# Kernel tuning notes

Measured on AMD Instinct MI355X. Metric: run time of the kernel, lower is better.

The kernel has to match this reference:

```python
import jax, jax.numpy as jnp
import numpy as np
from jax import lax

B, L, S = 32, 513, 1024
H, HEADS, NCLS = 512, 4, 128
SPACE, PAD, EOS = 1, 0, 2
WORD = 8                 # chunk: 7 phones + 1 space
WPB = (L - 1) // WORD    # words per batch = 64
TOTAL_WORDS = B * WPB    # 2048
WLEN = WORD - 1          # 7


def setup_inputs() -> dict:
    key = jax.random.key(0)
    ks = jax.random.split(key, 22)
    # targets: phones in [3, NCLS), every WORD-th token after position 0 is SPACE; no EOS/PAD
    tg = np.array(jax.random.randint(ks[0], (B, L), 3, NCLS))
    t = np.arange(1, L)
    col = tg[:, 1:]
    col[:, (t - 1) % WORD == WORD - 1] = SPACE
    tg[:, 1:] = col
    targets = jnp.asarray(tg, dtype=jnp.int32)
    sc = 0.02
    p = lambda k, shape: jax.random.normal(k, shape, jnp.float32) * sc
    return dict(
        targets=targets,
        encoder_outputs=jax.random.normal(ks[1], (B, S, H), jnp.float32),
        emb_w=p(ks[2], (NCLS, H)),
        w_ih0=p(ks[3], (4 * H, H)), w_hh0=p(ks[4], (4 * H, H)),
        b_ih0=p(ks[5], (4 * H,)), b_hh0=p(ks[6], (4 * H,)),
        w_ih1=p(ks[7], (4 * H, H)), w_hh1=p(ks[8], (4 * H, H)),
        b_ih1=p(ks[9], (4 * H,)), b_hh1=p(ks[10], (4 * H,)),
        q_w=p(ks[11], (H, H)), q_b=p(ks[12], (H,)),
        k_w=p(ks[13], (H, H)), k_b=p(ks[14], (H,)),
        v_w=p(ks[15], (H, H)), v_b=p(ks[16], (H,)),
        fc1_w=p(ks[17], (H, 2 * H)), fc1_b=p(ks[18], (H,)),
        fc2_w=p(ks[19], (NCLS, H)), fc2_b=p(ks[20], (NCLS,)),
    )


def lstm_layer(x, w_ih, w_hh, b_ih, b_hh):
    # PyTorch LSTM, gate order (i, f, g, o), batch_first
    Bx, _, _ = x.shape
    Hh = w_hh.shape[1]
    xp = jnp.einsum('bth,gh->btg', x, w_ih) + b_ih + b_hh  # [B,T,4H]
    def step(carry, xt):
        h, c = carry
        g = xt + h @ w_hh.T
        i, f, gg, o = jnp.split(g, 4, axis=-1)
        c = jax.nn.sigmoid(f) * c + jax.nn.sigmoid(i) * jnp.tanh(gg)
        h = jax.nn.sigmoid(o) * jnp.tanh(c)
        return (h, c), h
    init = (jnp.zeros((Bx, Hh), x.dtype), jnp.zeros((Bx, Hh), x.dtype))
    _, hs = lax.scan(step, init, xp.transpose(1, 0, 2))
    return hs.transpose(1, 0, 2)


def mha(q_in, kv, q_w, q_b, k_w, k_b, v_w, v_b):
    dh = H // HEADS
    q = (q_in @ q_w.T + q_b).reshape(B, -1, HEADS, dh)
    k = (kv @ k_w.T + k_b).reshape(B, -1, HEADS, dh)
    v = (kv @ v_w.T + v_b).reshape(B, -1, HEADS, dh)
    scores = jnp.einsum('bqhd,bkhd->bhqk', q, k) / jnp.sqrt(jnp.float32(dh))
    attn = jax.nn.softmax(scores, axis=-1)
    ctx = jnp.einsum('bhqk,bkhd->bqhd', attn, v).reshape(B, -1, H)
    return ctx, attn


def split_words(ids, feat):
    # vectorized _split_output_to_word: segment-ids + scatter instead of python loops
    T = ids.shape[1]
    D = feat.shape[-1]
    boundary = (ids == SPACE) | (ids == PAD)          # word delimiters
    word_id = jnp.cumsum(boundary, axis=1) - boundary  # exclusive cumsum
    tpos = jnp.arange(T)
    seed = jnp.where(boundary, tpos + 1, 0)
    start = jnp.concatenate([jnp.zeros((B, 1), seed.dtype), lax.cummax(seed, axis=1)[:, :-1]], axis=1)
    pos = jnp.clip(tpos - start, 0, WLEN - 1)          # position within word
    gidx = jnp.where(boundary, TOTAL_WORDS, jnp.arange(B)[:, None] * WPB + word_id)
    out = jnp.zeros((TOTAL_WORDS + 1, WLEN, D), feat.dtype)
    out = out.at[gidx.ravel(), pos.ravel()].set(feat.reshape(-1, D))
    return out[:TOTAL_WORDS]  # [2048, 7, 2H]; all words length WLEN so torch zero-pad is a no-op


def reference(targets, encoder_outputs, emb_w, w_ih0, w_hh0, b_ih0, b_hh0, w_ih1, w_hh1, b_ih1, b_hh1, q_w, q_b, k_w, k_b, v_w, v_b, fc1_w, fc1_b, fc2_w, fc2_b):
    input_rnn = targets  # targets contain no eos by construction, so the eos-filter view is identity
    embedded = emb_w[input_rnn]  # input_dropout is identity in eval mode
    x = lstm_layer(embedded, w_ih0, w_hh0, b_ih0, b_hh0)
    outputs = lstm_layer(x, w_ih1, w_hh1, b_ih1, b_hh1)
    context, attn = mha(outputs, encoder_outputs, q_w, q_b, k_w, k_b, v_w, v_b)
    feat = jnp.concatenate([embedded[:, 1:], context[:, :-1]], axis=-1)  # [B, L-1, 2H]
    mis = split_words(input_rnn[:, 1:], feat)
    cat = jnp.concatenate([outputs, context], axis=-1)  # [B, L, 2H]
    h1 = jnp.tanh(cat @ fc1_w.T + fc1_b)
    logits = h1 @ fc2_w.T + fc2_b
    logp = jax.nn.log_softmax(logits, axis=-1)  # [B, L, NCLS]
    return logp, attn, mis
```

## Files before the change

### kernel.cpp

```cpp
#include <hip/hip_runtime.h>


typedef __attribute__((ext_vector_type(8))) short bf16x8;
typedef __attribute__((ext_vector_type(4))) float f32x4;

union U128 { unsigned long long q[2]; bf16x8 v; };

__device__ __forceinline__ unsigned short f2bf(float f) {
  union { float f; unsigned int u; } v; v.f = f;
  unsigned int r = (v.u + 0x7fffu + ((v.u >> 16) & 1u)) >> 16;
  return (unsigned short)r;
}
__device__ __forceinline__ float bf2f(unsigned short h) {
  union { unsigned int u; float f; } v; v.u = ((unsigned int)h) << 16;
  return v.f;
}

__device__ __forceinline__ unsigned long long ld_dev(const unsigned short* p) {
  return __hip_atomic_load((const unsigned long long*)p, __ATOMIC_RELAXED,
                           __HIP_MEMORY_SCOPE_AGENT);
}
__device__ __forceinline__ void st_dev(unsigned short* p, unsigned long long x) {
  __hip_atomic_store((unsigned long long*)p, x, __ATOMIC_RELAXED,
                     __HIP_MEMORY_SCOPE_AGENT);
}

typedef const __attribute__((address_space(1))) void* gp1_t;
typedef __attribute__((address_space(3))) void* lp3_t;
__device__ __forceinline__ void glds16(const void* g, void* s) {
  __builtin_amdgcn_global_load_lds((gp1_t)g, (lp3_t)s, 16, 0, 0);
}

struct Gemm {
  const unsigned short* A; const unsigned short* W; const float* bias;
  float* C1; unsigned short* C2;
  long lda, ldw, ldc1, ldc2;
  long zA, zAh, zW, zWh, zC1, zC1h, zC2, zC2h;
  long M, Mclamp;
  int N, K, heads, act;
  float alpha;
};

__global__ __launch_bounds__(256, 2) void gemm_bt(Gemm g) {
  __shared__ unsigned short aSh[128 * 32];
  __shared__ unsigned short bSh[128 * 32];
  const int tid = threadIdx.x;
  const int wave = tid >> 6, lane = tid & 63;
  const int zb = blockIdx.z / g.heads, zh = blockIdx.z % g.heads;
  const unsigned short* A = g.A + (long)zb * g.zA + (long)zh * g.zAh;
  const unsigned short* W = g.W + (long)zb * g.zW + (long)zh * g.zWh;
  const long mBlk = (long)blockIdx.y * 128;
  const long nBlk = (long)blockIdx.x * 128;
  const int sRow = wave * 16 + (lane >> 2);
  const int sCol = (lane & 3) * 8;
  long ar0 = mBlk + sRow;      if (ar0 > g.Mclamp) ar0 = g.Mclamp;
  long ar1 = mBlk + 64 + sRow; if (ar1 > g.Mclamp) ar1 = g.Mclamp;
  const unsigned short* gA0 = A + ar0 * g.lda + sCol;
  const unsigned short* gA1 = A + ar1 * g.lda + sCol;
  const unsigned short* gW0 = W + (nBlk + sRow) * g.ldw + sCol;
  const unsigned short* gW1 = W + (nBlk + 64 + sRow) * g.ldw + sCol;
  unsigned short* sA0 = aSh + wave * 512;
  unsigned short* sA1 = aSh + 2048 + wave * 512;
  unsigned short* sB0 = bSh + wave * 512;
  unsigned short* sB1 = bSh + 2048 + wave * 512;
  f32x4 acc[4][4] = {};
  const int wm = wave & 1, wn = wave >> 1;
  const int fm = lane & 15, fq = lane >> 4;
  for (int k0 = 0; k0 < g.K; k0 += 32) {
    glds16(gA0 + k0, sA0);
    glds16(gA1 + k0, sA1);
    glds16(gW0 + k0, sB0);
    glds16(gW1 + k0, sB1);
    __syncthreads();
    bf16x8 af[4], bfr[4];
#pragma unroll
    for (int i = 0; i < 4; ++i)
      af[i] = *(const bf16x8*)(aSh + (wm * 64 + i * 16 + fm) * 32 + fq * 8);
#pragma unroll
    for (int j = 0; j < 4; ++j)
      bfr[j] = *(const bf16x8*)(bSh + (wn * 64 + j * 16 + fm) * 32 + fq * 8);
#pragma unroll
    for (int i = 0; i < 4; ++i)
#pragma unroll
      for (int j = 0; j < 4; ++j)
        acc[i][j] = __builtin_amdgcn_mfma_f32_16x16x32_bf16(af[i], bfr[j], acc[i][j], 0, 0, 0);
    __syncthreads();
  }
  float* C1 = g.C1 ? g.C1 + (long)zb * g.zC1 + (long)zh * g.zC1h : nullptr;
  unsigned short* C2 = g.C2 ? g.C2 + (long)zb * g.zC2 + (long)zh * g.zC2h : nullptr;
#pragma unroll
  for (int j = 0; j < 4; ++j) {
    long n = nBlk + wn * 64 + j * 16 + fm;
    float bias = g.bias ? g.bias[n] : 0.f;
#pragma unroll
    for (int i = 0; i < 4; ++i) {
      long mBase = mBlk + wm * 64 + i * 16 + fq * 4;
#pragma unroll
      for (int r = 0; r < 4; ++r) {
        long m = mBase + r;
        if (m < g.M) {
          float v = acc[i][j][r] * g.alpha + bias;
          if (g.act) v = tanhf(v);
          if (C1) C1[m * g.ldc1 + n] = v;
          if (C2) C2[m * g.ldc2 + n] = f2bf(v);
        }
      }
    }
  }
}

__global__ __launch_bounds__(256, 1) void lstm_fused(
    const float* __restrict__ xp,
    const unsigned short* __restrict__ wih1,
    const unsigned short* __restrict__ whh0,
    const unsigned short* __restrict__ whh1,
    const float* __restrict__ bias1,
    unsigned short* __restrict__ h0,
    unsigned short* __restrict__ h1,
    unsigned int* bar) {
  __shared__ unsigned short wSh[2 * 16 * 520];
  __shared__ float gS[1056];
  __shared__ __align__(16) unsigned short hStage[256];
  const int tid = threadIdx.x, lane = tid & 63, wave = tid >> 6;
  const int bx = blockIdx.x;
  const int fm = lane & 15, fq = lane >> 4;

  if (bx < 64) {
    const int j0 = bx * 8;
    {
      const int row = tid >> 3, cb = (tid & 7) * 64;
      const unsigned short* wsrc =
          whh0 + ((long)((row >> 3) * 512 + j0 + (row & 7))) * 512 + cb;
      unsigned short* dst = wSh + row * 520 + cb;
#pragma unroll
      for (int c = 0; c < 64; c += 8) *(bf16x8*)(dst + c) = *(const bf16x8*)(wsrc + c);
    }
    __syncthreads();
    const int wm = wave & 1, wn = wave >> 1;
    const unsigned short* wrow = wSh + (wn * 16 + fm) * 520 + fq * 8;
    const long ab = wm * 16 + fm;
    const int cb2 = tid >> 3, jl = tid & 7;
    const float* xpp = xp + (long)cb2 * 513 * 2048 + j0 + jl;
    float cSt = 0.f;
    for (int r = 0; r < 514; ++r) {
      if (r < 513) {
        const int t = r;
        const float* xq = xpp + (long)t * 2048;
        float x0 = xq[0], x1 = xq[512], x2 = xq[1024], x3 = xq[1536];
        f32x4 acc = {0.f, 0.f, 0.f, 0.f};
        if (t > 0) {
          U128 afr[16];
          const unsigned short* hr = h0 + (ab * 513 + (t - 1)) * 512 + fq * 8;
#pragma unroll
          for (int kk = 0; kk < 16; ++kk) {
            afr[kk].q[0] = ld_dev(hr + kk * 32);
            afr[kk].q[1] = ld_dev(hr + kk * 32 + 4);
          }
#pragma unroll
          for (int kk = 0; kk < 16; ++kk)
            acc = __builtin_amdgcn_mfma_f32_16x16x32_bf16(
                afr[kk].v, *(const bf16x8*)(wrow + kk * 32), acc, 0, 0, 0);
        }
#pragma unroll
        for (int rr = 0; rr < 4; ++rr)
          gS[(wn * 16 + fm) * 33 + wm * 16 + fq * 4 + rr] = acc[rr];
        __syncthreads();
        {
          float gi = gS[jl * 33 + cb2] + x0;
          float gf = gS[(8 + jl) * 33 + cb2] + x1;
          float gg = gS[(16 + jl) * 33 + cb2] + x2;
          float go = gS[(24 + jl) * 33 + cb2] + x3;
          float ig = 1.f / (1.f + __expf(-gi));
          float fg = 1.f / (1.f + __expf(-gf));
          float og = 1.f / (1.f + __expf(-go));
          cSt = fg * cSt + ig * tanhf(gg);
          hStage[tid] = f2bf(og * tanhf(cSt));
        }
        __syncthreads();
        if (tid < 64) {
          const int b2 = tid >> 1, half = tid & 1;
          unsigned long long q = *(const unsigned long long*)(hStage + b2 * 8 + half * 4);
          st_dev(h0 + ((long)b2 * 513 + t) * 512 + j0 + half * 4, q);
        }
      }
      if (r < 513) {
        __syncthreads();
        if (tid == 0) {
          __hip_atomic_fetch_add(bar + (bx & 7) * 1024, 1u, __ATOMIC_RELAXED,
                                 __HIP_MEMORY_SCOPE_AGENT);
          const unsigned int tgt = 192u * (unsigned)(r + 1);
          for (;;) {
            unsigned int s = 0;
#pragma unroll
            for (int i = 0; i < 8; ++i)
              s += __hip_atomic_load(bar + i * 1024, __ATOMIC_RELAXED,
                                     __HIP_MEMORY_SCOPE_AGENT);
            if (s >= tgt) break;
            __builtin_amdgcn_s_sleep(1);
          }
        }
        __syncthreads();
      }
    }
  } else {
    const int j0 = (bx - 64) * 4;
    {
      const int mat = tid >> 7, row = (tid >> 3) & 15, cb = (tid & 7) * 64;
      const unsigned short* wsrc = (mat ? whh1 : wih1) +
          ((long)((row >> 2) * 512 + j0 + (row & 3))) * 512 + cb;
      unsigned short* dst = wSh + (mat * 16 + row) * 520 + cb;
#pragma unroll
      for (int c = 0; c < 64; c += 8) *(bf16x8*)(dst + c) = *(const bf16x8*)(wsrc + c);
    }
    __syncthreads();
    const int wm = wave & 1, ws = wave >> 1;
    const unsigned short* wrow = wSh + (ws * 16 + fm) * 520 + fq * 8;
    const long ab = wm * 16 + fm;
    const int cb2 = tid >> 2, jl = tid & 3;
    float bv0 = 0.f, bv1 = 0.f, bv2 = 0.f, bv3 = 0.f;
    if (tid < 128) {
      bv0 = bias1[j0 + jl];
      bv1 = bias1[512 + j0 + jl];
      bv2 = bias1[1024 + j0 + jl];
      bv3 = bias1[1536 + j0 + jl];
    }
    float cSt = 0.f;
    for (int r = 0; r < 514; ++r) {
      if (r >= 1) {
        const int t = r - 1;
        f32x4 acc = {0.f, 0.f, 0.f, 0.f};
        if (ws == 0 || t > 0) {
          U128 afr[16];
          const unsigned short* hr = (ws == 0)
              ? h0 + (ab * 513 + t) * 512 + fq * 8
              : h1 + (ab * 513 + (t - 1)) * 1024 + fq * 8;
#pragma unroll
          for (int kk = 0; kk < 16; ++kk) {
            afr[kk].q[0] = ld_dev(hr + kk * 32);
            afr[kk].q[1] = ld_dev(hr + kk * 32 + 4);
          }
#pragma unroll
          for (int kk = 0; kk < 16; ++kk)
            acc = __builtin_amdgcn_mfma_f32_16x16x32_bf16(
                afr[kk].v, *(const bf16x8*)(wrow + kk * 32), acc, 0, 0, 0);
        }
#pragma unroll
        for (int rr = 0; rr < 4; ++rr)
          gS[(ws * 16 + fm) * 33 + wm * 16 + fq * 4 + rr] = acc[rr];
        __syncthreads();
        if (tid < 128) {
          float gi = gS[jl * 33 + cb2]        + gS[(16 + jl) * 33 + cb2] + bv0;
          float gf = gS[(4 + jl) * 33 + cb2]  + gS[(20 + jl) * 33 + cb2] + bv1;
          float gg = gS[(8 + jl) * 33 + cb2]  + gS[(24 + jl) * 33 + cb2] + bv2;
          float go = gS[(12 + jl) * 33 + cb2] + gS[(28 + jl) * 33 + cb2] + bv3;
          float ig = 1.f / (1.f + __expf(-gi));
          float fg = 1.f / (1.f + __expf(-gf));
          float og = 1.f / (1.f + __expf(-go));
          cSt = fg * cSt + ig * tanhf(gg);
          hStage[tid] = f2bf(og * tanhf(cSt));
        }
        __syncthreads();
        if (tid < 32) {
          unsigned long long q = *(const unsigned long long*)(hStage + tid * 4);
          st_dev(h1 + ((long)tid * 513 + t) * 1024 + j0, q);
        }
      }
      if (r < 513) {
        __syncthreads();
        if (tid == 0) {
          __hip_atomic_fetch_add(bar + (bx & 7) * 1024, 1u, __ATOMIC_RELAXED,
                                 __HIP_MEMORY_SCOPE_AGENT);
          const unsigned int tgt = 192u * (unsigned)(r + 1);
          for (;;) {
            unsigned int s = 0;
#pragma unroll
            for (int i = 0; i < 8; ++i)
              s += __hip_atomic_load(bar + i * 1024, __ATOMIC_RELAXED,
                                     __HIP_MEMORY_SCOPE_AGENT);
            if (s >= tgt) break;
            __builtin_amdgcn_s_sleep(1);
          }
        }
        __syncthreads();
      }
    }
  }
}


struct CastJob { const float* src; unsigned short* dst; long n; };
struct CastJobs { CastJob j[11]; };
__global__ void cast_multi(CastJobs jb) {
  const CastJob j = jb.j[blockIdx.z];
  long n4 = j.n >> 2;
  for (long i = blockIdx.x * (long)blockDim.x + threadIdx.x; i < n4;
       i += (long)gridDim.x * blockDim.x) {
    float4 f = ((const float4*)j.src)[i];
    ushort4 o;
    o.x = f2bf(f.x); o.y = f2bf(f.y); o.z = f2bf(f.z); o.w = f2bf(f.w);
    ((ushort4*)j.dst)[i] = o;
  }
}

__global__ void bias_sum(const float* a0, const float* b0, float* o0,
                         const float* a1, const float* b1, float* o1) {
  int i = blockIdx.x * 256 + threadIdx.x;
  if (i < 2048) { o0[i] = a0[i] + b0[i]; o1[i] = a1[i] + b1[i]; }
}

__global__ __launch_bounds__(256) void embed_gather(const int* __restrict__ tg,
                                                    const unsigned short* __restrict__ emb,
                                                    unsigned short* __restrict__ out) {
  long row = blockIdx.x;
  int id = tg[row];
  const unsigned short* s = emb + (long)id * 512;
  unsigned short* d = out + row * 512;
  int c = threadIdx.x * 2;
  *(ushort2*)(d + c) = *(const ushort2*)(s + c);
}

__global__ void word_map(const int* __restrict__ tg, int* __restrict__ map) {
  int b = threadIdx.x;
  if (b >= 32) return;
  int word_id = 0, start = 0;
  for (int i = 0; i < 512; ++i) {
    int id = tg[b * 513 + i + 1];
    bool bd = (id == 1) || (id == 0);
    if (bd) {
      map[b * 512 + i] = -1;
      word_id++; start = i + 1;
    } else {
      int pos = i - start; if (pos > 6) pos = 6;
      map[b * 512 + i] = (b * 64 + word_id) * 7 + pos;
    }
  }
}

__global__ __launch_bounds__(256) void vtrans(const unsigned short* __restrict__ v,
                                              unsigned short* __restrict__ vt) {
  __shared__ unsigned short tile[64][33];
  const int bh = blockIdx.z, b = bh >> 2, h = bh & 3;
  const int s0 = blockIdx.x * 64, d0 = blockIdx.y * 32;
  const int tid = threadIdx.x;
  {
    const int dd = tid & 31, sb = tid >> 5;
#pragma unroll
    for (int k = 0; k < 8; ++k) {
      int s = sb + k * 8;
      tile[s][dd] = v[((long)b * 1024 + s0 + s) * 512 + h * 128 + d0 + dd];
    }
  }
  __syncthreads();
  {
    const int ss = tid & 63, db = tid >> 6;
#pragma unroll
    for (int k = 0; k < 8; ++k) {
      int d = db + k * 4;
      vt[((long)bh * 128 + d0 + d) * 1024 + s0 + ss] = tile[ss][d];
    }
  }
}

__global__ __launch_bounds__(256) void softmax_row(unsigned short* __restrict__ sc,
                                                   float* __restrict__ attnOut) {
  const long row = blockIdx.x;
  unsigned short* sr = sc + row * 1024;
  const int tid = threadIdx.x, lane = tid & 63, wave = tid >> 6;
  __shared__ float red[8];
  ushort4 raw = *(const ushort4*)(sr + tid * 4);
  float v0 = bf2f(raw.x), v1 = bf2f(raw.y), v2 = bf2f(raw.z), v3 = bf2f(raw.w);
  float m = fmaxf(fmaxf(v0, v1), fmaxf(v2, v3));
  for (int o = 32; o; o >>= 1) m = fmaxf(m, __shfl_down(m, o));
  if (lane == 0) red[wave] = m;
  __syncthreads();
  m = fmaxf(fmaxf(red[0], red[1]), fmaxf(red[2], red[3]));
  float e0 = __expf(v0 - m), e1 = __expf(v1 - m), e2 = __expf(v2 - m), e3 = __expf(v3 - m);
  float s = e0 + e1 + e2 + e3;
  for (int o = 32; o; o >>= 1) s += __shfl_down(s, o);
  if (lane == 0) red[4 + wave] = s;
  __syncthreads();
  float inv = 1.f / (red[4] + red[5] + red[6] + red[7]);
  float a0 = e0 * inv, a1 = e1 * inv, a2 = e2 * inv, a3 = e3 * inv;
  float4 fo; fo.x = a0; fo.y = a1; fo.z = a2; fo.w = a3;
  *(float4*)(attnOut + row * 1024 + tid * 4) = fo;
  ushort4 ob; ob.x = f2bf(a0); ob.y = f2bf(a1); ob.z = f2bf(a2); ob.w = f2bf(a3);
  *(ushort4*)(sr + tid * 4) = ob;
}

__global__ __launch_bounds__(128) void mis_scatter(const int* __restrict__ map,
                                                   const int* __restrict__ tg,
                                                   const float* __restrict__ emb_w,
                                                   const float* __restrict__ ctx,
                                                   float* __restrict__ mis) {
  int bi = blockIdx.x;
  int g = map[bi];
  if (g < 0) return;
  int b = bi >> 9, i = bi & 511;
  float* dst = mis + (long)g * 1024;
  int id = tg[b * 513 + i + 1];
  const float* es = emb_w + (long)id * 512;
  const float* cs = ctx + ((long)b * 513 + i) * 512;
  for (int c = threadIdx.x; c < 512; c += 128) {
    dst[c] = es[c];
    dst[512 + c] = cs[c];
  }
}

__global__ __launch_bounds__(256) void logsoftmax_rows(const float* __restrict__ logits,
                                                       float* __restrict__ out) {
  int row = blockIdx.x * 4 + (threadIdx.x >> 6);
  if (row >= 16416) return;
  int lane = threadIdx.x & 63;
  const float* lr = logits + (long)row * 128;
  float a = lr[lane], b = lr[lane + 64];
  float m = fmaxf(a, b);
  for (int o = 32; o; o >>= 1) m = fmaxf(m, __shfl_down(m, o));
  m = __shfl(m, 0);
  float s = __expf(a - m) + __expf(b - m);
  for (int o = 32; o; o >>= 1) s += __shfl_down(s, o);
  s = __shfl(s, 0);
  float ls = m + __logf(s);
  out[(long)row * 128 + lane] = a - ls;
  out[(long)row * 128 + lane + 64] = b - ls;
}


extern "C" void kernel_launch(void* const* d_in, const int* in_sizes, int n_in,
                              void* d_out, int out_size, void* d_ws, size_t ws_size,
                              hipStream_t stream) {
  (void)in_sizes; (void)n_in; (void)out_size; (void)ws_size;
  const int*   targets = (const int*)d_in[0];
  const float* enc   = (const float*)d_in[1];
  const float* emb_w = (const float*)d_in[2];
  const float* w_ih0 = (const float*)d_in[3];
  const float* w_hh0 = (const float*)d_in[4];
  const float* b_ih0 = (const float*)d_in[5];
  const float* b_hh0 = (const float*)d_in[6];
  const float* w_ih1 = (const float*)d_in[7];
  const float* w_hh1 = (const float*)d_in[8];
  const float* b_ih1 = (const float*)d_in[9];
  const float* b_hh1 = (const float*)d_in[10];
  const float* q_w = (const float*)d_in[11]; const float* q_b = (const float*)d_in[12];
  const float* k_w = (const float*)d_in[13]; const float* k_b = (const float*)d_in[14];
  const float* v_w = (const float*)d_in[15]; const float* v_b = (const float*)d_in[16];
  const float* fc1_w = (const float*)d_in[17]; const float* fc1_b = (const float*)d_in[18];
  const float* fc2_w = (const float*)d_in[19]; const float* fc2_b = (const float*)d_in[20];

  float* out_logp = (float*)d_out;
  float* out_attn = out_logp + 2101248;
  float* out_mis  = out_logp + 69341184;

  char* ws = (char*)d_ws;
  size_t off = 0;
  auto take = [&](size_t bytes) -> char* {
    char* p = ws + off; off += (bytes + 255) & ~(size_t)255; return p;
  };
  unsigned int* bar   = (unsigned int*)take(65536);
  int* map            = (int*)take(65536);
  float* bias0        = (float*)take(8192);
  float* bias1        = (float*)take(8192);
  unsigned short* wih0b = (unsigned short*)take(2097152);
  unsigned short* whh0b = (unsigned short*)take(2097152);
  unsigned short* wih1b = (unsigned short*)take(2097152);
  unsigned short* whh1b = (unsigned short*)take(2097152);
  unsigned short* qwb   = (unsigned short*)take(524288);
  unsigned short* kwb   = (unsigned short*)take(524288);
  unsigned short* vwb   = (unsigned short*)take(524288);
  unsigned short* fc1wb = (unsigned short*)take(1048576);
  unsigned short* fc2wb = (unsigned short*)take(131072);
  unsigned short* embb  = (unsigned short*)take(131072);
  unsigned short* emb_bf = (unsigned short*)take(16908288);
  unsigned short* enc_bf = (unsigned short*)take(33554432);
  float* xp             = (float*)take(135266304);
  unsigned short* scores = (unsigned short*)xp;
  unsigned short* h0_bf = (unsigned short*)take(16908288);
  unsigned short* cat_bf = (unsigned short*)take(33816576);
  unsigned short* q_bf  = (unsigned short*)take(16908288);
  unsigned short* k_bf  = (unsigned short*)take(33554432);
  unsigned short* v_bf  = (unsigned short*)take(33554432);
  unsigned short* v_t   = (unsigned short*)take(33554432);
  float* ctx            = (float*)take(33816576);
  unsigned short* h1_bf = (unsigned short*)take(16908288);
  float* logits         = (float*)take(8454144);

  hipMemsetAsync(bar, 0, 32768, stream);
  hipMemsetAsync(out_mis, 0, (size_t)14680064 * 4, stream);

  CastJobs cj;
  cj.j[0]  = {w_ih0, wih0b, 1048576};
  cj.j[1]  = {w_hh0, whh0b, 1048576};
  cj.j[2]  = {w_ih1, wih1b, 1048576};
  cj.j[3]  = {w_hh1, whh1b, 1048576};
  cj.j[4]  = {q_w,   qwb,   262144};
  cj.j[5]  = {k_w,   kwb,   262144};
  cj.j[6]  = {v_w,   vwb,   262144};
  cj.j[7]  = {fc1_w, fc1wb, 524288};
  cj.j[8]  = {fc2_w, fc2wb, 65536};
  cj.j[9]  = {emb_w, embb,  65536};
  cj.j[10] = {enc,   enc_bf, 16777216};
  cast_multi<<<dim3(256, 1, 11), 256, 0, stream>>>(cj);
  bias_sum<<<8, 256, 0, stream>>>(b_ih0, b_hh0, bias0, b_ih1, b_hh1, bias1);
  word_map<<<1, 64, 0, stream>>>(targets, map);
  embed_gather<<<16416, 256, 0, stream>>>(targets, embb, emb_bf);

  auto launch_gemm = [&](const unsigned short* A, long lda, long zA, long zAh,
                         const unsigned short* W, long ldw, long zW, long zWh,
                         const float* bias, float* C1, long ldc1, long zC1, long zC1h,
                         unsigned short* C2, long ldc2, long zC2, long zC2h,
                         long M, long Mclamp, int N, int K, int heads, int Z,
                         float alpha, int act) {
    Gemm g;
    g.A = A; g.W = W; g.bias = bias; g.C1 = C1; g.C2 = C2;
    g.lda = lda; g.ldw = ldw; g.ldc1 = ldc1; g.ldc2 = ldc2;
    g.zA = zA; g.zAh = zAh; g.zW = zW; g.zWh = zWh;
    g.zC1 = zC1; g.zC1h = zC1h; g.zC2 = zC2; g.zC2h = zC2h;
    g.M = M; g.Mclamp = Mclamp; g.N = N; g.K = K; g.heads = heads;
    g.act = act; g.alpha = alpha;
    dim3 grid((unsigned)(N / 128), (unsigned)((M + 127) / 128), (unsigned)Z);
    gemm_bt<<<grid, 256, 0, stream>>>(g);
  };

  launch_gemm(emb_bf, 512, 0, 0, wih0b, 512, 0, 0, bias0,
              xp, 2048, 0, 0, nullptr, 0, 0, 0,
              16512, 16511, 2048, 512, 1, 1, 1.f, 0);
  lstm_fused<<<192, 256, 0, stream>>>(xp, wih1b, whh0b, whh1b, bias1,
                                      h0_bf, cat_bf, bar);

  launch_gemm(cat_bf, 1024, 0, 0, qwb, 512, 0, 0, q_b,
              nullptr, 0, 0, 0, q_bf, 512, 0, 0,
              16512, 16511, 512, 512, 1, 1, 1.f, 0);
  launch_gemm(enc_bf, 512, 0, 0, kwb, 512, 0, 0, k_b,
              nullptr, 0, 0, 0, k_bf, 512, 0, 0,
              32768, 32767, 512, 512, 1, 1, 1.f, 0);
  launch_gemm(enc_bf, 512, 0, 0, vwb, 512, 0, 0, v_b,
              nullptr, 0, 0, 0, v_bf, 512, 0, 0,
              32768, 32767, 512, 512, 1, 1, 1.f, 0);
  vtrans<<<dim3(16, 4, 128), 256, 0, stream>>>(v_bf, v_t);

  launch_gemm(q_bf, 512, 262656, 128, k_bf, 512, 524288, 128, nullptr,
              nullptr, 0, 0, 0, scores, 1024, 2101248, 525312,
              513, 512, 1024, 128, 4, 128, 0.08838834764831845f, 0);
  softmax_row<<<65664, 256, 0, stream>>>(scores, out_attn);
  launch_gemm(scores, 1024, 2101248, 525312, v_t, 1024, 524288, 131072, nullptr,
              ctx, 512, 262656, 128, cat_bf + 512, 1024, 525312, 128,
              513, 512, 128, 1024, 4, 128, 1.f, 0);
  mis_scatter<<<16384, 128, 0, stream>>>(map, targets, emb_w, ctx, out_mis);

  launch_gemm(cat_bf, 1024, 0, 0, fc1wb, 1024, 0, 0, fc1_b,
              nullptr, 0, 0, 0, h1_bf, 512, 0, 0,
              16512, 16511, 512, 1024, 1, 1, 1.f, 1);
  launch_gemm(h1_bf, 512, 0, 0, fc2wb, 512, 0, 0, fc2_b,
              logits, 128, 0, 0, nullptr, 0, 0, 0,
              16512, 16511, 128, 512, 1, 1, 1.f, 0);
  logsoftmax_rows<<<4104, 256, 0, stream>>>(logits, out_logp);
}
```

Before: 4.035 ms.

## Restructure fused LSTM into 48 blocks with register weights and per-block flags

The persistent two-layer LSTM kernel drops from 192 to 48 blocks. Each wave now holds its weight fragments in registers instead of LDS and computes all four gates for its hidden slice, so the gate nonlinearity runs straight from the MFMA accumulators without an LDS transpose. The global counting barrier is replaced by per-block progress flags. Layer 0 waits only on layer-0 blocks, and layer 1 waits on layer-0 step t and layer-1 step t-1, which lets the two layers pipeline instead of moving in lockstep. The cost is heavy register pressure from 64 bf16x8 fragments per thread and fewer CUs doing the serial work.

```diff
diff --git a/kernel.cpp b/kernel.cpp
--- a/kernel.cpp
+++ b/kernel.cpp
@@ -5,6 +5,7 @@
 typedef __attribute__((ext_vector_type(4))) float f32x4;
 
 union U128 { unsigned long long q[2]; bf16x8 v; };
+union HV { ushort4 u; unsigned long long q; };
 
 __device__ __forceinline__ unsigned short f2bf(float f) {
   union { float f; unsigned int u; } v; v.f = f;
@@ -23,6 +24,12 @@
 __device__ __forceinline__ void st_dev(unsigned short* p, unsigned long long x) {
   __hip_atomic_store((unsigned long long*)p, x, __ATOMIC_RELAXED,
                      __HIP_MEMORY_SCOPE_AGENT);
+}
+__device__ __forceinline__ unsigned int ld_flag(const unsigned int* p) {
+  return __hip_atomic_load(p, __ATOMIC_RELAXED, __HIP_MEMORY_SCOPE_AGENT);
+}
+__device__ __forceinline__ void st_flag(unsigned int* p, unsigned int v) {
+  __hip_atomic_store(p, v, __ATOMIC_RELAXED, __HIP_MEMORY_SCOPE_AGENT);
 }
 
 typedef const __attribute__((address_space(1))) void* gp1_t;
@@ -118,171 +125,182 @@
     unsigned short* __restrict__ h0,
     unsigned short* __restrict__ h1,
     unsigned int* bar) {
-  __shared__ unsigned short wSh[2 * 16 * 520];
-  __shared__ float gS[1056];
-  __shared__ __align__(16) unsigned short hStage[256];
+  __shared__ float xch[16 * 128];
   const int tid = threadIdx.x, lane = tid & 63, wave = tid >> 6;
+  const int fm = lane & 15, fq = lane >> 4;
   const int bx = blockIdx.x;
-  const int fm = lane & 15, fq = lane >> 4;
-
-  if (bx < 64) {
-    const int j0 = bx * 8;
-    {
-      const int row = tid >> 3, cb = (tid & 7) * 64;
-      const unsigned short* wsrc =
-          whh0 + ((long)((row >> 3) * 512 + j0 + (row & 7))) * 512 + cb;
-      unsigned short* dst = wSh + row * 520 + cb;
-#pragma unroll
-      for (int c = 0; c < 64; c += 8) *(bf16x8*)(dst + c) = *(const bf16x8*)(wsrc + c);
-    }
-    __syncthreads();
-    const int wm = wave & 1, wn = wave >> 1;
-    const unsigned short* wrow = wSh + (wn * 16 + fm) * 520 + fq * 8;
-    const long ab = wm * 16 + fm;
-    const int cb2 = tid >> 3, jl = tid & 7;
-    const float* xpp = xp + (long)cb2 * 513 * 2048 + j0 + jl;
-    float cSt = 0.f;
-    for (int r = 0; r < 514; ++r) {
-      if (r < 513) {
-        const int t = r;
-        const float* xq = xpp + (long)t * 2048;
-        float x0 = xq[0], x1 = xq[512], x2 = xq[1024], x3 = xq[1536];
-        f32x4 acc = {0.f, 0.f, 0.f, 0.f};
-        if (t > 0) {
-          U128 afr[16];
-          const unsigned short* hr = h0 + (ab * 513 + (t - 1)) * 512 + fq * 8;
-#pragma unroll
-          for (int kk = 0; kk < 16; ++kk) {
-            afr[kk].q[0] = ld_dev(hr + kk * 32);
-            afr[kk].q[1] = ld_dev(hr + kk * 32 + 4);
+
+  if (bx < 16) {
+    const int j0 = bx * 32;
+    const int m = wave & 1, p = wave >> 1;
+    const int b = m * 16 + fm;
+    const int c0 = p * 16 + fq * 4;
+    bf16x8 wf[4][16];
+#pragma unroll
+    for (int g = 0; g < 4; ++g) {
+      const unsigned short* wr =
+          whh0 + ((long)(g * 512 + j0 + p * 16 + fm)) * 512 + fq * 8;
+#pragma unroll
+      for (int kk = 0; kk < 16; ++kk)
+        wf[g][kk] = *(const bf16x8*)(wr + kk * 32);
+    }
+    const float* xpt = xp + ((long)b * 513) * 2048 + j0 + c0;
+    unsigned short* hout = h0 + ((long)b * 513) * 512 + j0 + c0;
+    const unsigned short* hin = h0 + ((long)b * 513) * 512 + fq * 8;
+    float cS[4] = {0.f, 0.f, 0.f, 0.f};
+#pragma unroll 1
+    for (int t = 0; t < 513; ++t) {
+      const float4 xi = *(const float4*)(xpt + (long)t * 2048);
+      const float4 xf = *(const float4*)(xpt + (long)t * 2048 + 512);
+      const float4 xg = *(const float4*)(xpt + (long)t * 2048 + 1024);
+      const float4 xo = *(const float4*)(xpt + (long)t * 2048 + 1536);
+      if (tid == 0 && t > 0) {
+        for (;;) {
+          unsigned int mn = ~0u;
+#pragma unroll
+          for (int i = 0; i < 16; ++i) {
+            unsigned int v = ld_flag(bar + i * 16);
+            mn = v < mn ? v : mn;
           }
-#pragma unroll
-          for (int kk = 0; kk < 16; ++kk)
-            acc = __builtin_amdgcn_mfma_f32_16x16x32_bf16(
-                afr[kk].v, *(const bf16x8*)(wrow + kk * 32), acc, 0, 0, 0);
-        }
-#pragma unroll
-        for (int rr = 0; rr < 4; ++rr)
-          gS[(wn * 16 + fm) * 33 + wm * 16 + fq * 4 + rr] = acc[rr];
-        __syncthreads();
-        {
-          float gi = gS[jl * 33 + cb2] + x0;
-          float gf = gS[(8 + jl) * 33 + cb2] + x1;
-          float gg = gS[(16 + jl) * 33 + cb2] + x2;
-          float go = gS[(24 + jl) * 33 + cb2] + x3;
+          if (mn >= (unsigned int)t) break;
+          __builtin_amdgcn_s_sleep(1);
+        }
+      }
+      __syncthreads();
+      f32x4 a0 = {}, a1 = {}, a2 = {}, a3 = {};
+      if (t > 0) {
+        U128 hf[16];
+        const unsigned short* hr = hin + (long)(t - 1) * 512;
+#pragma unroll
+        for (int kk = 0; kk < 16; ++kk) {
+          hf[kk].q[0] = ld_dev(hr + kk * 32);
+          hf[kk].q[1] = ld_dev(hr + kk * 32 + 4);
+        }
+#pragma unroll
+        for (int kk = 0; kk < 16; ++kk) {
+          a0 = __builtin_amdgcn_mfma_f32_16x16x32_bf16(wf[0][kk], hf[kk].v, a0, 0, 0, 0);
+          a1 = __builtin_amdgcn_mfma_f32_16x16x32_bf16(wf[1][kk], hf[kk].v, a1, 0, 0, 0);
+          a2 = __builtin_amdgcn_mfma_f32_16x16x32_bf16(wf[2][kk], hf[kk].v, a2, 0, 0, 0);
+          a3 = __builtin_amdgcn_mfma_f32_16x16x32_bf16(wf[3][kk], hf[kk].v, a3, 0, 0, 0);
+        }
+      }
+      const float xiv[4] = {xi.x, xi.y, xi.z, xi.w};
+      const float xfv[4] = {xf.x, xf.y, xf.z, xf.w};
+      const float xgv[4] = {xg.x, xg.y, xg.z, xg.w};
+      const float xov[4] = {xo.x, xo.y, xo.z, xo.w};
+      unsigned short hh[4];
+#pragma unroll
+      for (int rr = 0; rr < 4; ++rr) {
+        float gi = a0[rr] + xiv[rr];
+        float gf = a1[rr] + xfv[rr];
+        float gg = a2[rr] + xgv[rr];
+        float go = a3[rr] + xov[rr];
+        float ig = 1.f / (1.f + __expf(-gi));
+        float fg = 1.f / (1.f + __expf(-gf));
+        float og = 1.f / (1.f + __expf(-go));
+        cS[rr] = fg * cS[rr] + ig * tanhf(gg);
+        hh[rr] = f2bf(og * tanhf(cS[rr]));
+      }
+      HV hv; hv.u.x = hh[0]; hv.u.y = hh[1]; hv.u.z = hh[2]; hv.u.w = hh[3];
+      st_dev(hout + (long)t * 512, hv.q);
+      __syncthreads();
+      if (tid == 0) st_flag(bar + bx * 16, (unsigned int)(t + 1));
+    }
+  } else {
+    const int blk = bx - 16, j0 = blk * 16;
+    const int m = wave & 1, part = wave >> 1;
+    const int b = m * 16 + fm;
+    const int c0 = fq * 4;
+    bf16x8 wf[4][16];
+    const unsigned short* wmat = part ? whh1 : wih1;
+#pragma unroll
+    for (int g = 0; g < 4; ++g) {
+      const unsigned short* wr =
+          wmat + ((long)(g * 512 + j0 + fm)) * 512 + fq * 8;
+#pragma unroll
+      for (int kk = 0; kk < 16; ++kk)
+        wf[g][kk] = *(const bf16x8*)(wr + kk * 32);
+    }
+    float bias_r[4][4];
+    if (part == 0) {
+#pragma unroll
+      for (int g = 0; g < 4; ++g) {
+        float4 bg = *(const float4*)(bias1 + g * 512 + j0 + c0);
+        bias_r[g][0] = bg.x; bias_r[g][1] = bg.y;
+        bias_r[g][2] = bg.z; bias_r[g][3] = bg.w;
+      }
+    }
+    const unsigned short* h0in = h0 + ((long)b * 513) * 512 + fq * 8;
+    const unsigned short* h1in = h1 + ((long)b * 513) * 1024 + fq * 8;
+    unsigned short* hout = h1 + ((long)b * 513) * 1024 + j0 + c0;
+    float cS[4] = {0.f, 0.f, 0.f, 0.f};
+#pragma unroll 1
+    for (int t = 0; t < 513; ++t) {
+      if (tid == 0) {
+        for (;;) {
+          unsigned int mnA = ~0u, mnB = ~0u;
+#pragma unroll
+          for (int i = 0; i < 16; ++i) {
+            unsigned int v = ld_flag(bar + i * 16);
+            mnA = v < mnA ? v : mnA;
+          }
+#pragma unroll
+          for (int j = 0; j < 32; ++j) {
+            unsigned int v = ld_flag(bar + (16 + j) * 16);
+            mnB = v < mnB ? v : mnB;
+          }
+          if (mnA >= (unsigned int)(t + 1) && mnB >= (unsigned int)t) break;
+          __builtin_amdgcn_s_sleep(1);
+        }
+      }
+      __syncthreads();
+      f32x4 a0 = {}, a1 = {}, a2 = {}, a3 = {};
+      if (part == 0 || t > 0) {
+        const unsigned short* hr = (part == 0) ? h0in + (long)t * 512
+                                               : h1in + (long)(t - 1) * 1024;
+        U128 hf[16];
+#pragma unroll
+        for (int kk = 0; kk < 16; ++kk) {
+          hf[kk].q[0] = ld_dev(hr + kk * 32);
+          hf[kk].q[1] = ld_dev(hr + kk * 32 + 4);
+        }
+#pragma unroll
+        for (int kk = 0; kk < 16; ++kk) {
+          a0 = __builtin_amdgcn_mfma_f32_16x16x32_bf16(wf[0][kk], hf[kk].v, a0, 0, 0, 0);
+          a1 = __builtin_amdgcn_mfma_f32_16x16x32_bf16(wf[1][kk], hf[kk].v, a1, 0, 0, 0);
+          a2 = __builtin_amdgcn_mfma_f32_16x16x32_bf16(wf[2][kk], hf[kk].v, a2, 0, 0, 0);
+          a3 = __builtin_amdgcn_mfma_f32_16x16x32_bf16(wf[3][kk], hf[kk].v, a3, 0, 0, 0);
+        }
+      }
+      if (part == 1) {
+#pragma unroll
+        for (int rr = 0; rr < 4; ++rr) {
+          xch[(0 * 4 + rr) * 128 + m * 64 + lane] = a0[rr];
+          xch[(1 * 4 + rr) * 128 + m * 64 + lane] = a1[rr];
+          xch[(2 * 4 + rr) * 128 + m * 64 + lane] = a2[rr];
+          xch[(3 * 4 + rr) * 128 + m * 64 + lane] = a3[rr];
+        }
+      }
+      __syncthreads();
+      if (part == 0) {
+        unsigned short hh[4];
+#pragma unroll
+        for (int rr = 0; rr < 4; ++rr) {
+          float gi = a0[rr] + xch[(0 * 4 + rr) * 128 + m * 64 + lane] + bias_r[0][rr];
+          float gf = a1[rr] + xch[(1 * 4 + rr) * 128 + m * 64 + lane] + bias_r[1][rr];
+          float gg = a2[rr] + xch[(2 * 4 + rr) * 128 + m * 64 + lane] + bias_r[2][rr];
+          float go = a3[rr] + xch[(3 * 4 + rr) * 128 + m * 64 + lane] + bias_r[3][rr];
           float ig = 1.f / (1.f + __expf(-gi));
           float fg = 1.f / (1.f + __expf(-gf));
           float og = 1.f / (1.f + __expf(-go));
-          cSt = fg * cSt + ig * tanhf(gg);
-          hStage[tid] = f2bf(og * tanhf(cSt));
-        }
-        __syncthreads();
-        if (tid < 64) {
-          const int b2 = tid >> 1, half = tid & 1;
-          unsigned long long q = *(const unsigned long long*)(hStage + b2 * 8 + half * 4);
-          st_dev(h0 + ((long)b2 * 513 + t) * 512 + j0 + half * 4, q);
-        }
-      }
-      if (r < 513) {
-        __syncthreads();
-        if (tid == 0) {
-          __hip_atomic_fetch_add(bar + (bx & 7) * 1024, 1u, __ATOMIC_RELAXED,
-                                 __HIP_MEMORY_SCOPE_AGENT);
-          const unsigned int tgt = 192u * (unsigned)(r + 1);
-          for (;;) {
-            unsigned int s = 0;
-#pragma unroll
-            for (int i = 0; i < 8; ++i)
-              s += __hip_atomic_load(bar + i * 1024, __ATOMIC_RELAXED,
-                                     __HIP_MEMORY_SCOPE_AGENT);
-            if (s >= tgt) break;
-            __builtin_amdgcn_s_sleep(1);
-          }
-        }
-        __syncthreads();
-      }
-    }
-  } else {
-    const int j0 = (bx - 64) * 4;
-    {
-      const int mat = tid >> 7, row = (tid >> 3) & 15, cb = (tid & 7) * 64;
-      const unsigned short* wsrc = (mat ? whh1 : wih1) +
-          ((long)((row >> 2) * 512 + j0 + (row & 3))) * 512 + cb;
-      unsigned short* dst = wSh + (mat * 16 + row) * 520 + cb;
-#pragma unroll
-      for (int c = 0; c < 64; c += 8) *(bf16x8*)(dst + c) = *(const bf16x8*)(wsrc + c);
-    }
-    __syncthreads();
-    const int wm = wave & 1, ws = wave >> 1;
-    const unsigned short* wrow = wSh + (ws * 16 + fm) * 520 + fq * 8;
-    const long ab = wm * 16 + fm;
-    const int cb2 = tid >> 2, jl = tid & 3;
-    float bv0 = 0.f, bv1 = 0.f, bv2 = 0.f, bv3 = 0.f;
-    if (tid < 128) {
-      bv0 = bias1[j0 + jl];
-      bv1 = bias1[512 + j0 + jl];
-      bv2 = bias1[1024 + j0 + jl];
-      bv3 = bias1[1536 + j0 + jl];
-    }
-    float cSt = 0.f;
-    for (int r = 0; r < 514; ++r) {
-      if (r >= 1) {
-        const int t = r - 1;
-        f32x4 acc = {0.f, 0.f, 0.f, 0.f};
-        if (ws == 0 || t > 0) {
-          U128 afr[16];
-          const unsigned short* hr = (ws == 0)
-              ? h0 + (ab * 513 + t) * 512 + fq * 8
-              : h1 + (ab * 513 + (t - 1)) * 1024 + fq * 8;
-#pragma unroll
-          for (int kk = 0; kk < 16; ++kk) {
-            afr[kk].q[0] = ld_dev(hr + kk * 32);
-            afr[kk].q[1] = ld_dev(hr + kk * 32 + 4);
-          }
-#pragma unroll
-          for (int kk = 0; kk < 16; ++kk)
-            acc = __builtin_amdgcn_mfma_f32_16x16x32_bf16(
-                afr[kk].v, *(const bf16x8*)(wrow + kk * 32), acc, 0, 0, 0);
-        }
-#pragma unroll
-        for (int rr = 0; rr < 4; ++rr)
-          gS[(ws * 16 + fm) * 33 + wm * 16 + fq * 4 + rr] = acc[rr];
-        __syncthreads();
-        if (tid < 128) {
-          float gi = gS[jl * 33 + cb2]        + gS[(16 + jl) * 33 + cb2] + bv0;
-          float gf = gS[(4 + jl) * 33 + cb2]  + gS[(20 + jl) * 33 + cb2] + bv1;
-          float gg = gS[(8 + jl) * 33 + cb2]  + gS[(24 + jl) * 33 + cb2] + bv2;
-          float go = gS[(12 + jl) * 33 + cb2] + gS[(28 + jl) * 33 + cb2] + bv3;
-          float ig = 1.f / (1.f + __expf(-gi));
-          float fg = 1.f / (1.f + __expf(-gf));
-          float og = 1.f / (1.f + __expf(-go));
-          cSt = fg * cSt + ig * tanhf(gg);
-          hStage[tid] = f2bf(og * tanhf(cSt));
-        }
-        __syncthreads();
-        if (tid < 32) {
-          unsigned long long q = *(const unsigned long long*)(hStage + tid * 4);
-          st_dev(h1 + ((long)tid * 513 + t) * 1024 + j0, q);
-        }
-      }
-      if (r < 513) {
-        __syncthreads();
-        if (tid == 0) {
-          __hip_atomic_fetch_add(bar + (bx & 7) * 1024, 1u, __ATOMIC_RELAXED,
-                                 __HIP_MEMORY_SCOPE_AGENT);
-          const unsigned int tgt = 192u * (unsigned)(r + 1);
-          for (;;) {
-            unsigned int s = 0;
-#pragma unroll
-            for (int i = 0; i < 8; ++i)
-              s += __hip_atomic_load(bar + i * 1024, __ATOMIC_RELAXED,
-                                     __HIP_MEMORY_SCOPE_AGENT);
-            if (s >= tgt) break;
-            __builtin_amdgcn_s_sleep(1);
-          }
-        }
-        __syncthreads();
-      }
+          cS[rr] = fg * cS[rr] + ig * tanhf(gg);
+          hh[rr] = f2bf(og * tanhf(cS[rr]));
+        }
+        HV hv; hv.u.x = hh[0]; hv.u.y = hh[1]; hv.u.z = hh[2]; hv.u.w = hh[3];
+        st_dev(hout + (long)t * 1024, hv.q);
+      }
+      __syncthreads();
+      if (tid == 0) st_flag(bar + (16 + blk) * 16, (unsigned int)(t + 1));
     }
   }
 }
@@ -523,8 +541,8 @@
   launch_gemm(emb_bf, 512, 0, 0, wih0b, 512, 0, 0, bias0,
               xp, 2048, 0, 0, nullptr, 0, 0, 0,
               16512, 16511, 2048, 512, 1, 1, 1.f, 0);
-  lstm_fused<<<192, 256, 0, stream>>>(xp, wih1b, whh0b, whh1b, bias1,
-                                      h0_bf, cat_bf, bar);
+  lstm_fused<<<48, 256, 0, stream>>>(xp, wih1b, whh0b, whh1b, bias1,
+                                     h0_bf, cat_bf, bar);
 
   launch_gemm(cat_bf, 1024, 0, 0, qwb, 512, 0, 0, q_b,
               nullptr, 0, 0, 0, q_bf, 512, 0, 0,
```

Result: slower. 6.808 ms (+68.7%).

## Replace global counting barrier with per-block progress flags in persistent LSTM kernel

Applied to the files above, without the earlier changes.

The fused two-layer LSTM kernel previously stopped all 192 blocks at a global atomic counter barrier after every timestep. Each block now publishes its own progress flag. Layer-0 blocks wait only until all layer-0 blocks finish the previous step. Layer-1 blocks wait for the layer-0 flags of step t and the layer-1 flags of step t-1, with the min taken by a wave-wide shuffle reduction. This cuts atomic contention and lets the two layers run pipelined rather than in lockstep. It relies on relaxed atomics plus __syncthreads for memory ordering, which may be fragile, and it needs the bar buffer zeroed with a stride-16 layout.

```diff
diff --git a/kernel.cpp b/kernel.cpp
--- a/kernel.cpp
+++ b/kernel.cpp
@@ -23,6 +23,12 @@
 __device__ __forceinline__ void st_dev(unsigned short* p, unsigned long long x) {
   __hip_atomic_store((unsigned long long*)p, x, __ATOMIC_RELAXED,
                      __HIP_MEMORY_SCOPE_AGENT);
+}
+__device__ __forceinline__ unsigned int ld_flag(const unsigned int* p) {
+  return __hip_atomic_load(p, __ATOMIC_RELAXED, __HIP_MEMORY_SCOPE_AGENT);
+}
+__device__ __forceinline__ void st_flag(unsigned int* p, unsigned int v) {
+  __hip_atomic_store(p, v, __ATOMIC_RELAXED, __HIP_MEMORY_SCOPE_AGENT);
 }
 
 typedef const __attribute__((address_space(1))) void* gp1_t;
@@ -142,65 +148,60 @@
     const int cb2 = tid >> 3, jl = tid & 7;
     const float* xpp = xp + (long)cb2 * 513 * 2048 + j0 + jl;
     float cSt = 0.f;
-    for (int r = 0; r < 514; ++r) {
-      if (r < 513) {
-        const int t = r;
-        const float* xq = xpp + (long)t * 2048;
-        float x0 = xq[0], x1 = xq[512], x2 = xq[1024], x3 = xq[1536];
-        f32x4 acc = {0.f, 0.f, 0.f, 0.f};
-        if (t > 0) {
-          U128 afr[16];
-          const unsigned short* hr = h0 + (ab * 513 + (t - 1)) * 512 + fq * 8;
-#pragma unroll
-          for (int kk = 0; kk < 16; ++kk) {
-            afr[kk].q[0] = ld_dev(hr + kk * 32);
-            afr[kk].q[1] = ld_dev(hr + kk * 32 + 4);
-          }
-#pragma unroll
-          for (int kk = 0; kk < 16; ++kk)
-            acc = __builtin_amdgcn_mfma_f32_16x16x32_bf16(
-                afr[kk].v, *(const bf16x8*)(wrow + kk * 32), acc, 0, 0, 0);
-        }
-#pragma unroll
-        for (int rr = 0; rr < 4; ++rr)
-          gS[(wn * 16 + fm) * 33 + wm * 16 + fq * 4 + rr] = acc[rr];
-        __syncthreads();
-        {
-          float gi = gS[jl * 33 + cb2] + x0;
-          float gf = gS[(8 + jl) * 33 + cb2] + x1;
-          float gg = gS[(16 + jl) * 33 + cb2] + x2;
-          float go = gS[(24 + jl) * 33 + cb2] + x3;
-          float ig = 1.f / (1.f + __expf(-gi));
-          float fg = 1.f / (1.f + __expf(-gf));
-          float og = 1.f / (1.f + __expf(-go));
-          cSt = fg * cSt + ig * tanhf(gg);
-          hStage[tid] = f2bf(og * tanhf(cSt));
+#pragma unroll 1
+    for (int t = 0; t < 513; ++t) {
+      const float* xq = xpp + (long)t * 2048;
+      float x0 = xq[0], x1 = xq[512], x2 = xq[1024], x3 = xq[1536];
+      if (t > 0) {
+        if (wave == 0) {
+          int mn;
+          do {
+            int v = (int)ld_flag(bar + lane * 16);
+#pragma unroll
+            for (int o = 32; o; o >>= 1) { int u = __shfl_xor(v, o); v = u < v ? u : v; }
+            mn = v;
+            if (mn < t) __builtin_amdgcn_s_sleep(1);
+          } while (mn < t);
         }
         __syncthreads();
-        if (tid < 64) {
-          const int b2 = tid >> 1, half = tid & 1;
-          unsigned long long q = *(const unsigned long long*)(hStage + b2 * 8 + half * 4);
-          st_dev(h0 + ((long)b2 * 513 + t) * 512 + j0 + half * 4, q);
+      }
+      f32x4 acc = {0.f, 0.f, 0.f, 0.f};
+      if (t > 0) {
+        U128 afr[16];
+        const unsigned short* hr = h0 + (ab * 513 + (t - 1)) * 512 + fq * 8;
+#pragma unroll
+        for (int kk = 0; kk < 16; ++kk) {
+          afr[kk].q[0] = ld_dev(hr + kk * 32);
+          afr[kk].q[1] = ld_dev(hr + kk * 32 + 4);
         }
-      }
-      if (r < 513) {
-        __syncthreads();
-        if (tid == 0) {
-          __hip_atomic_fetch_add(bar + (bx & 7) * 1024, 1u, __ATOMIC_RELAXED,
-                                 __HIP_MEMORY_SCOPE_AGENT);
-          const unsigned int tgt = 192u * (unsigned)(r + 1);
-          for (;;) {
-            unsigned int s = 0;
-#pragma unroll
-            for (int i = 0; i < 8; ++i)
-              s += __hip_atomic_load(bar + i * 1024, __ATOMIC_RELAXED,
-                                     __HIP_MEMORY_SCOPE_AGENT);
-            if (s >= tgt) break;
-            __builtin_amdgcn_s_sleep(1);
-          }
-        }
-        __syncthreads();
-      }
+#pragma unroll
+        for (int kk = 0; kk < 16; ++kk)
+          acc = __builtin_amdgcn_mfma_f32_16x16x32_bf16(
+              afr[kk].v, *(const bf16x8*)(wrow + kk * 32), acc, 0, 0, 0);
+      }
+#pragma unroll
+      for (int rr = 0; rr < 4; ++rr)
+        gS[(wn * 16 + fm) * 33 + wm * 16 + fq * 4 + rr] = acc[rr];
+      __syncthreads();
+      {
+        float gi = gS[jl * 33 + cb2] + x0;
+        float gf = gS[(8 + jl) * 33 + cb2] + x1;
+        float gg = gS[(16 + jl) * 33 + cb2] + x2;
+        float go = gS[(24 + jl) * 33 + cb2] + x3;
+        float ig = 1.f / (1.f + __expf(-gi));
+        float fg = 1.f / (1.f + __expf(-gf));
+        float og = 1.f / (1.f + __expf(-go));
+        cSt = fg * cSt + ig * tanhf(gg);
+        hStage[tid] = f2bf(og * tanhf(cSt));
+      }
+      __syncthreads();
+      if (tid < 64) {
+        const int b2 = tid >> 1, half = tid & 1;
+        unsigned long long q = *(const unsigned long long*)(hStage + b2 * 8 + half * 4);
+        st_dev(h0 + ((long)b2 * 513 + t) * 512 + j0 + half * 4, q);
+      }
+      __syncthreads();
+      if (tid == 0) st_flag(bar + bx * 16, (unsigned int)(t + 1));
     }
   } else {
     const int j0 = (bx - 64) * 4;
@@ -225,64 +226,61 @@
       bv3 = bias1[1536 + j0 + jl];
     }
     float cSt = 0.f;
-    for (int r = 0; r < 514; ++r) {
-      if (r >= 1) {
-        const int t = r - 1;
-        f32x4 acc = {0.f, 0.f, 0.f, 0.f};
-        if (ws == 0 || t > 0) {
-          U128 afr[16];
-          const unsigned short* hr = (ws == 0)
-              ? h0 + (ab * 513 + t) * 512 + fq * 8
-              : h1 + (ab * 513 + (t - 1)) * 1024 + fq * 8;
-#pragma unroll
-          for (int kk = 0; kk < 16; ++kk) {
-            afr[kk].q[0] = ld_dev(hr + kk * 32);
-            afr[kk].q[1] = ld_dev(hr + kk * 32 + 4);
-          }
-#pragma unroll
-          for (int kk = 0; kk < 16; ++kk)
-            acc = __builtin_amdgcn_mfma_f32_16x16x32_bf16(
-                afr[kk].v, *(const bf16x8*)(wrow + kk * 32), acc, 0, 0, 0);
+#pragma unroll 1
+    for (int t = 0; t < 513; ++t) {
+      if (wave == 0) {
+        int mn;
+        do {
+          int v0 = (int)ld_flag(bar + lane * 16);
+          int v1 = (int)ld_flag(bar + (64 + lane) * 16);
+          int v2 = (int)ld_flag(bar + (128 + lane) * 16);
+          int v = (v1 < v2 ? v1 : v2) + 1;
+          v = v0 < v ? v0 : v;
+#pragma unroll
+          for (int o = 32; o; o >>= 1) { int u = __shfl_xor(v, o); v = u < v ? u : v; }
+          mn = v;
+          if (mn < t + 1) __builtin_amdgcn_s_sleep(1);
+        } while (mn < t + 1);
+      }
+      __syncthreads();
+      f32x4 acc = {0.f, 0.f, 0.f, 0.f};
+      if (ws == 0 || t > 0) {
+        const unsigned short* hr = (ws == 0)
+            ? h0 + (ab * 513 + t) * 512 + fq * 8
+            : h1 + (ab * 513 + (t - 1)) * 1024 + fq * 8;
+        U128 hf[16];
+#pragma unroll
+        for (int kk = 0; kk < 16; ++kk) {
+          hf[kk].q[0] = ld_dev(hr + kk * 32);
+          hf[kk].q[1] = ld_dev(hr + kk * 32 + 4);
         }
 #pragma unroll
-        for (int rr = 0; rr < 4; ++rr)
-          gS[(ws * 16 + fm) * 33 + wm * 16 + fq * 4 + rr] = acc[rr];
-        __syncthreads();
-        if (tid < 128) {
-          float gi = gS[jl * 33 + cb2]        + gS[(16 + jl) * 33 + cb2] + bv0;
-          float gf = gS[(4 + jl) * 33 + cb2]  + gS[(20 + jl) * 33 + cb2] + bv1;
-          float gg = gS[(8 + jl) * 33 + cb2]  + gS[(24 + jl) * 33 + cb2] + bv2;
-          float go = gS[(12 + jl) * 33 + cb2] + gS[(28 + jl) * 33 + cb2] + bv3;
-          float ig = 1.f / (1.f + __expf(-gi));
-          float fg = 1.f / (1.f + __expf(-gf));
-          float og = 1.f / (1.f + __expf(-go));
-          cSt = fg * cSt + ig * tanhf(gg);
-          hStage[tid] = f2bf(og * tanhf(cSt));
-        }
-        __syncthreads();
-        if (tid < 32) {
-          unsigned long long q = *(const unsigned long long*)(hStage + tid * 4);
-          st_dev(h1 + ((long)tid * 513 + t) * 1024 + j0, q);
-        }
-      }
-      if (r < 513) {
-        __syncthreads();
-        if (tid == 0) {
-          __hip_atomic_fetch_add(bar + (bx & 7) * 1024, 1u, __ATOMIC_RELAXED,
-                                 __HIP_MEMORY_SCOPE_AGENT);
-          const unsigned int tgt = 192u * (unsigned)(r + 1);
-          for (;;) {
-            unsigned int s = 0;
-#pragma unroll
-            for (int i = 0; i < 8; ++i)
-              s += __hip_atomic_load(bar + i * 1024, __ATOMIC_RELAXED,
-                                     __HIP_MEMORY_SCOPE_AGENT);
-            if (s >= tgt) break;
-            __builtin_amdgcn_s_sleep(1);
-          }
-        }
-        __syncthreads();
-      }
+        for (int kk = 0; kk < 16; ++kk)
+          acc = __builtin_amdgcn_mfma_f32_16x16x32_bf16(
+              hf[kk].v, *(const bf16x8*)(wrow + kk * 32), acc, 0, 0, 0);
+      }
+#pragma unroll
+      for (int rr = 0; rr < 4; ++rr)
+        gS[(ws * 16 + fm) * 33 + wm * 16 + fq * 4 + rr] = acc[rr];
+      __syncthreads();
+      if (tid < 128) {
+        float gi = gS[jl * 33 + cb2]        + gS[(16 + jl) * 33 + cb2] + bv0;
+        float gf = gS[(4 + jl) * 33 + cb2]  + gS[(20 + jl) * 33 + cb2] + bv1;
+        float gg = gS[(8 + jl) * 33 + cb2]  + gS[(24 + jl) * 33 + cb2] + bv2;
+        float go = gS[(12 + jl) * 33 + cb2] + gS[(28 + jl) * 33 + cb2] + bv3;
+        float ig = 1.f / (1.f + __expf(-gi));
+        float fg = 1.f / (1.f + __expf(-gf));
+        float og = 1.f / (1.f + __expf(-go));
+        cSt = fg * cSt + ig * tanhf(gg);
+        hStage[tid] = f2bf(og * tanhf(cSt));
+      }
+      __syncthreads();
+      if (tid < 32) {
+        unsigned long long q = *(const unsigned long long*)(hStage + tid * 4);
+        st_dev(h1 + ((long)tid * 513 + t) * 1024 + j0, q);
+      }
+      __syncthreads();
+      if (tid == 0) st_flag(bar + bx * 16, (unsigned int)(t + 1));
     }
   }
 }
```

Result: slower. 4.158 ms (+3.0%).
